# Kernel optimization log

Measured on AMD Instinct MI355X. Metric: run time of the kernel, lower is better.

## Reference

```python
import jax, jax.numpy as jnp
import numpy as np

EMBED_DIM = 1408
NUM_HEADS = 16
HEAD_DIM = EMBED_DIM // NUM_HEADS  # 88
SCALE = HEAD_DIM ** -0.5


def setup_inputs() -> dict:
    key = jax.random.key(0)
    k0, k1, k2, k3, k4 = jax.random.split(key, 5)
    B, S, D = 16, 577, EMBED_DIM
    hidden_states = jax.random.normal(k0, (B, S, D), dtype=jnp.float32)
    # fused QKV projection: [D, 3D] laid out as [q | k | v]
    w_qkv = jax.random.normal(k1, (D, 3 * D), dtype=jnp.float32) * (D ** -0.5)
    b_qkv = jax.random.normal(k2, (3 * D,), dtype=jnp.float32) * 0.02
    # output projection
    w_proj = jax.random.normal(k3, (D, D), dtype=jnp.float32) * (D ** -0.5)
    b_proj = jax.random.normal(k4, (D,), dtype=jnp.float32) * 0.02
    return {
        "hidden_states": hidden_states,
        "w_qkv": w_qkv,
        "b_qkv": b_qkv,
        "w_proj": w_proj,
        "b_proj": b_proj,
    }


def reference(hidden_states, w_qkv, b_qkv, w_proj, b_proj):
    B, S, D = hidden_states.shape
    H, Hd = NUM_HEADS, HEAD_DIM
    # fused QKV projection, then chunk along last dim (matches .chunk(3, -1))
    qkv = hidden_states @ w_qkv + b_qkv                      # [B, S, 3D]
    q, k, v = jnp.split(qkv, 3, axis=-1)                     # each [B, S, D]
    q = q.reshape(B, S, H, Hd)
    k = k.reshape(B, S, H, Hd)
    v = v.reshape(B, S, H, Hd)
    # scaled dot-product attention (no mask, no dropout at inference)
    scores = jnp.einsum("bqhd,bkhd->bhqk", q, k) * SCALE      # [B, H, S, S]
    probs = jax.nn.softmax(scores, axis=-1)
    out = jnp.einsum("bhqk,bkhd->bqhd", probs, v)             # [B, S, H, Hd]
    out = out.reshape(B, S, D)
    attn_output = out @ w_proj + b_proj                        # [B, S, D]
    return attn_output
```

## Files before the change

kernel.cpp:

```cpp
#include <hip/hip_runtime.h>
#include <cstddef>
#include <cstdint>

#define D_EMB   1408
#define NHEADS  16
#define HD      88
#define BATCH   16
#define SEQ     577
#define M_ROWS  (BATCH * SEQ)
#define N_QKV   (3 * D_EMB)
#define QKL_N   2816
#define SP      640
#define ATT_SCALE 0.10660035817780521f

#define QT 64
#define KT 64

typedef __attribute__((ext_vector_type(8))) short bf16x8;
typedef __attribute__((ext_vector_type(4))) float f32x4;
typedef unsigned short u16;

static __device__ __forceinline__ u16 f2bf(float x) {
  union { float f; unsigned u; } v; v.f = x;
  unsigned r = v.u + 0x7fff + ((v.u >> 16) & 1);
  return (u16)(r >> 16);
}
static __device__ __forceinline__ float bf2f(u16 h) {
  union { unsigned u; float f; } v; v.u = ((unsigned)h) << 16;
  return v.f;
}
static __device__ __forceinline__ void split_hl(float x, u16* hi, u16* lo) {
  u16 h = f2bf(x);
  *hi = h;
  *lo = f2bf(x - bf2f(h));
}

static __device__ __forceinline__ void async16(const u16* g, u16* l) {
  __builtin_amdgcn_global_load_lds(
      (const __attribute__((address_space(1))) unsigned int*)g,
      (__attribute__((address_space(3))) unsigned int*)l, 16, 0, 0);
}

__global__ __launch_bounds__(256)
void split_kernel(const float* __restrict__ X, u16* __restrict__ H,
                  u16* __restrict__ L, int n4) {
  int i = blockIdx.x * 256 + threadIdx.x;
  if (i >= n4) return;
  float4 v = ((const float4*)X)[i];
  ushort4 h, l;
  split_hl(v.x, &h.x, &l.x);
  split_hl(v.y, &h.y, &l.y);
  split_hl(v.z, &h.z, &l.z);
  split_hl(v.w, &h.w, &l.w);
  ((ushort4*)H)[i] = h;
  ((ushort4*)L)[i] = l;
}

__global__ __launch_bounds__(256)
void transpose_split_kernel(const float* __restrict__ W, u16* __restrict__ Th,
                            u16* __restrict__ Tl, int K, int N) {
  __shared__ float tile[32][33];
  const int n0 = blockIdx.x * 32, k0 = blockIdx.y * 32;
  const int tx = threadIdx.x & 31, ty = threadIdx.x >> 5;
#pragma unroll
  for (int i = 0; i < 4; ++i) {
    int k = ty + i * 8;
    tile[k][tx] = W[(size_t)(k0 + k) * N + n0 + tx];
  }
  __syncthreads();
#pragma unroll
  for (int i = 0; i < 4; ++i) {
    int n = ty + i * 8;
    float v = tile[tx][n];
    u16 h, l;
    split_hl(v, &h, &l);
    Th[(size_t)(n0 + n) * K + k0 + tx] = h;
    Tl[(size_t)(n0 + n) * K + k0 + tx] = l;
  }
}

__global__ __launch_bounds__(256)
void vtrans_kernel(const u16* __restrict__ qkvh, u16* __restrict__ vt) {
  __shared__ u16 tile[64][96];
  const int st = blockIdx.x, bh = blockIdx.y;
  const int b = bh >> 4, h = bh & 15;
  const int tid = threadIdx.x;
  const int s0 = st * 64;
  for (int idx = tid; idx < 64 * 22; idx += 256) {
    int j = idx / 22, c4 = (idx % 22) * 4;
    int s = s0 + j;
    ushort4 v = make_ushort4(0, 0, 0, 0);
    if (s < SEQ)
      v = *(const ushort4*)(qkvh + (size_t)(b * SEQ + s) * N_QKV + 2 * D_EMB + h * HD + c4);
    *(ushort4*)&tile[j][c4] = v;
  }
  if (tid < 64) {
    bf16x8 z = {0, 0, 0, 0, 0, 0, 0, 0};
    *(bf16x8*)&tile[tid][88] = z;
  }
  __syncthreads();
  for (int idx = tid; idx < 96 * 8; idx += 256) {
    int d = idx >> 3, c8 = (idx & 7) * 8;
    bf16x8 o;
#pragma unroll
    for (int e = 0; e < 8; ++e) o[e] = (short)tile[c8 + e][d];
    *(bf16x8*)(vt + ((size_t)bh * 96 + d) * SP + s0 + c8) = o;
  }
}

#define KDIM   1408
#define BMT    256
#define BNT    256
#define SLOT_E 32768
#define AS_H   0
#define AS_L   8192
#define BS_H   16384
#define BS_L   24576

#define STG_A(SLOTP, SSN)                                                 \
  {                                                                       \
    const int k0s = (SSN) * 32;                                           \
    u16* Ls = &Lds[SLOTP][0];                                             \
    async16(Ah + srcA0 + k0s, Ls + AS_H + ldsD0);                         \
    async16(Al + srcA0 + k0s, Ls + AS_L + ldsD0);                         \
    async16(Ah + srcA1 + k0s, Ls + AS_H + ldsD1);                         \
    async16(Al + srcA1 + k0s, Ls + AS_L + ldsD1);                         \
  }
#define STG_B(SLOTP, SSN)                                                 \
  {                                                                       \
    const int k0s = (SSN) * 32;                                           \
    u16* Ls = &Lds[SLOTP][0];                                             \
    async16(Bh + srcB0 + k0s, Ls + BS_H + ldsD0);                         \
    async16(Bl + srcB0 + k0s, Ls + BS_L + ldsD0);                         \
    async16(Bh + srcB1 + k0s, Ls + BS_H + ldsD1);                         \
    async16(Bl + srcB1 + k0s, Ls + BS_L + ldsD1);                         \
  }

#define MFMA3(ACC, AH, AL, BH, BL)                                                  \
  ACC = __builtin_amdgcn_mfma_f32_16x16x32_bf16(AH, BH, ACC, 0, 0, 0);              \
  ACC = __builtin_amdgcn_mfma_f32_16x16x32_bf16(AH, BL, ACC, 0, 0, 0);              \
  ACC = __builtin_amdgcn_mfma_f32_16x16x32_bf16(AL, BH, ACC, 0, 0, 0);

#define ROW_MFMA(I, AH, AL)                                               \
  MFMA3(acc[I][0], AH, AL, fbh0, fbl0)                                    \
  MFMA3(acc[I][1], AH, AL, fbh1, fbl1)                                    \
  MFMA3(acc[I][2], AH, AL, fbh2, fbl2)                                    \
  MFMA3(acc[I][3], AH, AL, fbh3, fbl3)

#define PH_SYNC                                                           \
  __builtin_amdgcn_s_barrier();                                           \
  asm volatile("s_waitcnt lgkmcnt(0)" ::: "memory");                      \
  __builtin_amdgcn_sched_barrier(0);

#define SLOT_RUN(PHYS, SSN, DO_STAGE, DO_VM)                              \
  {                                                                       \
    const u16* Lb = &Lds[PHYS][0];                                        \
    bf16x8 fbh0, fbh1, fbh2, fbh3, fbl0, fbl1, fbl2, fbl3;                \
    bf16x8 a0h, a0l, a1h, a1l;                                            \
                              \
    fbh0 = *(const bf16x8*)&Lb[BS_H + offB[0]];                           \
    fbh1 = *(const bf16x8*)&Lb[BS_H + offB[1]];                           \
    fbh2 = *(const bf16x8*)&Lb[BS_H + offB[2]];                           \
    fbh3 = *(const bf16x8*)&Lb[BS_H + offB[3]];                           \
    fbl0 = *(const bf16x8*)&Lb[BS_L + offB[0]];                           \
    fbl1 = *(const bf16x8*)&Lb[BS_L + offB[1]];                           \
    fbl2 = *(const bf16x8*)&Lb[BS_L + offB[2]];                           \
    fbl3 = *(const bf16x8*)&Lb[BS_L + offB[3]];                           \
    a0h = *(const bf16x8*)&Lb[AS_H + offA[0]];                            \
    a0l = *(const bf16x8*)&Lb[AS_L + offA[0]];                            \
    a1h = *(const bf16x8*)&Lb[AS_H + offA[1]];                            \
    a1l = *(const bf16x8*)&Lb[AS_L + offA[1]];                            \
    if (DO_STAGE) STG_A(PHYS ^ 1, SSN);                                   \
    PH_SYNC                                                               \
    __builtin_amdgcn_s_setprio(1);                                        \
    ROW_MFMA(0, a0h, a0l) ROW_MFMA(1, a1h, a1l)                           \
    __builtin_amdgcn_s_setprio(0);                                        \
    __builtin_amdgcn_s_barrier();                                         \
                                           \
    a0h = *(const bf16x8*)&Lb[AS_H + offA[2]];                            \
    a0l = *(const bf16x8*)&Lb[AS_L + offA[2]];                            \
    a1h = *(const bf16x8*)&Lb[AS_H + offA[3]];                            \
    a1l = *(const bf16x8*)&Lb[AS_L + offA[3]];                            \
    if (DO_STAGE) STG_B(PHYS ^ 1, SSN);                                   \
    PH_SYNC                                                               \
    __builtin_amdgcn_s_setprio(1);                                        \
    ROW_MFMA(2, a0h, a0l) ROW_MFMA(3, a1h, a1l)                           \
    __builtin_amdgcn_s_setprio(0);                                        \
    __builtin_amdgcn_s_barrier();                                         \
                                           \
    a0h = *(const bf16x8*)&Lb[AS_H + offA[4]];                            \
    a0l = *(const bf16x8*)&Lb[AS_L + offA[4]];                            \
    a1h = *(const bf16x8*)&Lb[AS_H + offA[5]];                            \
    a1l = *(const bf16x8*)&Lb[AS_L + offA[5]];                            \
    PH_SYNC                                                               \
    __builtin_amdgcn_s_setprio(1);                                        \
    ROW_MFMA(4, a0h, a0l) ROW_MFMA(5, a1h, a1l)                           \
    __builtin_amdgcn_s_setprio(0);                                        \
    __builtin_amdgcn_s_barrier();                                         \
                                           \
    a0h = *(const bf16x8*)&Lb[AS_H + offA[6]];                            \
    a0l = *(const bf16x8*)&Lb[AS_L + offA[6]];                            \
    a1h = *(const bf16x8*)&Lb[AS_H + offA[7]];                            \
    a1l = *(const bf16x8*)&Lb[AS_L + offA[7]];                            \
    PH_SYNC                                                               \
    __builtin_amdgcn_s_setprio(1);                                        \
    ROW_MFMA(6, a0h, a0l) ROW_MFMA(7, a1h, a1l)                           \
    __builtin_amdgcn_s_setprio(0);                                        \
    if (DO_VM) asm volatile("s_waitcnt vmcnt(0)" ::: "memory");           \
    __builtin_amdgcn_s_barrier();                                         \
  }

template <int MODE>
__global__ __launch_bounds__(512)
void gemm8p_kernel(const u16* __restrict__ Ah, const u16* __restrict__ Al,
                   const u16* __restrict__ Bh, const u16* __restrict__ Bl,
                   const float* __restrict__ bias,
                   float* __restrict__ Cf, u16* __restrict__ Ch, u16* __restrict__ Cl,
                   int M, int N, int NX) {
  const int lin  = blockIdx.x;
  const int xcd  = lin & 7;
  const int t    = lin >> 3;
  const int band = xcd + 8 * (t / NX);
  const int bm0  = band * BMT;
  if (bm0 >= M) return;
  const int bn0  = (t % NX) * BNT;

  __shared__ u16 Lds[2][SLOT_E];

  const int tid  = threadIdx.x;
  const int lane = tid & 63;
  const int w    = tid >> 6;
  const int quad = lane >> 4, lc = lane & 15;
  const int wm   = w >> 2, wn = w & 3;

  size_t srcA0, srcA1, srcB0, srcB1;
  int ldsD0, ldsD1;
  {
    int r0 = tid >> 2, q0 = tid & 3;
    int swz0 = (q0 ^ ((r0 >> 1) & 3)) * 8;
    int r1 = 128 + r0;
    int swz1 = (q0 ^ ((r1 >> 1) & 3)) * 8;
    int ra0 = bm0 + r0; if (ra0 > M - 1) ra0 = M - 1;
    int ra1 = bm0 + r1; if (ra1 > M - 1) ra1 = M - 1;
    srcA0 = (size_t)ra0 * KDIM + swz0;
    srcA1 = (size_t)ra1 * KDIM + swz1;
    int rb0 = bn0 + r0; if (rb0 > N - 1) rb0 = N - 1;
    int rb1 = bn0 + r1; if (rb1 > N - 1) rb1 = N - 1;
    srcB0 = (size_t)rb0 * KDIM + swz0;
    srcB1 = (size_t)rb1 * KDIM + swz1;
    ldsD0 = w * 512;
    ldsD1 = 4096 + w * 512;
  }

  int offA[8], offB[4];
  {
    const int qphys = quad ^ ((lc >> 1) & 3);
#pragma unroll
    for (int i = 0; i < 8; ++i)
      offA[i] = (wm * 128 + i * 16 + lc) * 32 + qphys * 8;
#pragma unroll
    for (int j = 0; j < 4; ++j)
      offB[j] = (wn * 64 + j * 16 + lc) * 32 + qphys * 8;
  }

  f32x4 acc[8][4];
#pragma unroll
  for (int i = 0; i < 8; ++i)
#pragma unroll
    for (int j = 0; j < 4; ++j) acc[i][j] = (f32x4){0.f, 0.f, 0.f, 0.f};

  STG_A(0, 0);
  STG_B(0, 0);
  asm volatile("s_waitcnt vmcnt(0)" ::: "memory");
  __builtin_amdgcn_s_barrier();

#pragma unroll 1
  for (int u = 0; u < 21; ++u) {
    SLOT_RUN(0, 2 * u + 1, true, true);
    SLOT_RUN(1, 2 * u + 2, true, true);
  }
  SLOT_RUN(0, 43, true, true);
  SLOT_RUN(1, 0, false, false);

#pragma unroll
  for (int j = 0; j < 4; ++j) {
    int col = bn0 + wn * 64 + j * 16 + lc;
    if (col < N) {
      float bj = bias[col];
#pragma unroll
      for (int i = 0; i < 8; ++i) {
#pragma unroll
        for (int rg = 0; rg < 4; ++rg) {
          int row = bm0 + wm * 128 + i * 16 + quad * 4 + rg;
          if (row < M) {
            float v = acc[i][j][rg] + bj;
            if (MODE == 0) {
              Cf[(size_t)row * N + col] = v;
            } else {
              u16 hh, ll;
              split_hl(v, &hh, &ll);
              Ch[(size_t)row * N + col] = hh;
              if (col < QKL_N) Cl[(size_t)row * QKL_N + col] = ll;
            }
          }
        }
      }
    }
  }
}

__global__ __launch_bounds__(256)
void attn_kernel2(const u16* __restrict__ qkvh, const u16* __restrict__ qkvl,
                  const u16* __restrict__ vt,
                  u16* __restrict__ outh, u16* __restrict__ outl) {
  __shared__ u16 Khi[KT][104];
  __shared__ u16 Klo[KT][104];
  __shared__ u16 Vs[96][72];
  __shared__ u16 Pb[QT][72];

  const int tid  = threadIdx.x;
  const int lane = tid & 63;
  const int wv   = tid >> 6;
  const int quad = lane >> 4;
  const int lc   = lane & 15;

  const int qt = blockIdx.x, h = blockIdx.y, b = blockIdx.z;
  const int q0 = qt * QT;

  if (tid < KT) {
    bf16x8 z = {0, 0, 0, 0, 0, 0, 0, 0};
    *(bf16x8*)&Khi[tid][88] = z;
    *(bf16x8*)&Klo[tid][88] = z;
  }

  bf16x8 qh[3], ql[3];
  {
    const bf16x8 z = {0, 0, 0, 0, 0, 0, 0, 0};
    int qrow = q0 + wv * 16 + lc;
    bool qv = qrow < SEQ;
    size_t bh_ = (size_t)(b * SEQ + (qv ? qrow : 0));
#pragma unroll
    for (int ks = 0; ks < 3; ++ks) {
      if (!qv || (ks == 2 && quad == 3)) {
        qh[ks] = z; ql[ks] = z;
      } else {
        qh[ks] = *(const bf16x8*)(qkvh + bh_ * N_QKV + h * HD + ks * 32 + quad * 8);
        ql[ks] = *(const bf16x8*)(qkvl + bh_ * QKL_N + h * HD + ks * 32 + quad * 8);
      }
    }
  }

  float mrow[4], lrow[4];
#pragma unroll
  for (int r = 0; r < 4; ++r) { mrow[r] = -INFINITY; lrow[r] = 0.f; }
  f32x4 oacc[6];
#pragma unroll
  for (int nn = 0; nn < 6; ++nn) oacc[nn] = (f32x4){0.f, 0.f, 0.f, 0.f};

  const u16* vsrc = vt + (size_t)(b * 16 + h) * 96 * SP;

  for (int kt = 0; kt < SP / KT; ++kt) {
    const int k0 = kt * KT;
    __syncthreads();

    for (int idx = tid; idx < KT * 22; idx += 256) {
      int j = idx / 22, c4 = (idx % 22) * 4;
      int s = k0 + j;
      ushort4 kh = make_ushort4(0, 0, 0, 0), kl = make_ushort4(0, 0, 0, 0);
      if (s < SEQ) {
        size_t rb = (size_t)(b * SEQ + s);
        kh = *(const ushort4*)(qkvh + rb * N_QKV + D_EMB + h * HD + c4);
        kl = *(const ushort4*)(qkvl + rb * QKL_N + D_EMB + h * HD + c4);
      }
      *(ushort4*)&Khi[j][c4] = kh;
      *(ushort4*)&Klo[j][c4] = kl;
    }
    for (int idx = tid; idx < 96 * 8; idx += 256) {
      int d = idx >> 3, c8 = (idx & 7) * 8;
      *(bf16x8*)&Vs[d][c8] = *(const bf16x8*)(vsrc + (size_t)d * SP + k0 + c8);
    }
    __syncthreads();

    f32x4 sc[4];
#pragma unroll
    for (int t = 0; t < 4; ++t) {
      f32x4 a = (f32x4){0.f, 0.f, 0.f, 0.f};
#pragma unroll
      for (int ks = 0; ks < 3; ++ks) {
        bf16x8 kh = *(const bf16x8*)&Khi[t * 16 + lc][ks * 32 + quad * 8];
        bf16x8 kl = *(const bf16x8*)&Klo[t * 16 + lc][ks * 32 + quad * 8];
        a = __builtin_amdgcn_mfma_f32_16x16x32_bf16(qh[ks], kh, a, 0, 0, 0);
        a = __builtin_amdgcn_mfma_f32_16x16x32_bf16(qh[ks], kl, a, 0, 0, 0);
        a = __builtin_amdgcn_mfma_f32_16x16x32_bf16(ql[ks], kh, a, 0, 0, 0);
      }
      sc[t] = a;
    }
#pragma unroll
    for (int t = 0; t < 4; ++t) {
      bool valid = (k0 + t * 16 + lc) < SEQ;
#pragma unroll
      for (int r = 0; r < 4; ++r)
        sc[t][r] = valid ? sc[t][r] * ATT_SCALE : -INFINITY;
    }

    float alpha[4];
#pragma unroll
    for (int r = 0; r < 4; ++r) {
      float v = fmaxf(fmaxf(sc[0][r], sc[1][r]), fmaxf(sc[2][r], sc[3][r]));
      v = fmaxf(v, __shfl_xor(v, 1));
      v = fmaxf(v, __shfl_xor(v, 2));
      v = fmaxf(v, __shfl_xor(v, 4));
      v = fmaxf(v, __shfl_xor(v, 8));
      float mnew = fmaxf(mrow[r], v);
      alpha[r] = expf(mrow[r] - mnew);
      mrow[r] = mnew;
      float s = 0.f;
#pragma unroll
      for (int t = 0; t < 4; ++t) {
        float p = expf(sc[t][r] - mnew);
        sc[t][r] = p;
        s += p;
      }
      s += __shfl_xor(s, 1);
      s += __shfl_xor(s, 2);
      s += __shfl_xor(s, 4);
      s += __shfl_xor(s, 8);
      lrow[r] = lrow[r] * alpha[r] + s;
    }
#pragma unroll
    for (int t = 0; t < 4; ++t)
#pragma unroll
      for (int r = 0; r < 4; ++r)
        Pb[wv * 16 + quad * 4 + r][t * 16 + lc] = f2bf(sc[t][r]);
#pragma unroll
    for (int nn = 0; nn < 6; ++nn)
#pragma unroll
      for (int r = 0; r < 4; ++r) oacc[nn][r] *= alpha[r];
    __syncthreads();

    bf16x8 p0 = *(const bf16x8*)&Pb[wv * 16 + lc][quad * 8];
    bf16x8 p1 = *(const bf16x8*)&Pb[wv * 16 + lc][32 + quad * 8];
#pragma unroll
    for (int nn = 0; nn < 6; ++nn) {
      bf16x8 v0 = *(const bf16x8*)&Vs[nn * 16 + lc][quad * 8];
      bf16x8 v1 = *(const bf16x8*)&Vs[nn * 16 + lc][32 + quad * 8];
      oacc[nn] = __builtin_amdgcn_mfma_f32_16x16x32_bf16(p0, v0, oacc[nn], 0, 0, 0);
      oacc[nn] = __builtin_amdgcn_mfma_f32_16x16x32_bf16(p1, v1, oacc[nn], 0, 0, 0);
    }
  }

#pragma unroll
  for (int r = 0; r < 4; ++r) {
    int s = q0 + wv * 16 + quad * 4 + r;
    if (s < SEQ) {
      float inv = 1.f / lrow[r];
      size_t base = (size_t)(b * SEQ + s) * D_EMB + h * HD;
#pragma unroll
      for (int nn = 0; nn < 6; ++nn) {
        int d = nn * 16 + lc;
        if (d < HD) {
          float v = oacc[nn][r] * inv;
          u16 hh, ll;
          split_hl(v, &hh, &ll);
          outh[base + d] = hh;
          outl[base + d] = ll;
        }
      }
    }
  }
}

extern "C" void kernel_launch(void* const* d_in, const int* in_sizes, int n_in,
                              void* d_out, int out_size, void* d_ws, size_t ws_size,
                              hipStream_t stream) {
  const float* hs    = (const float*)d_in[0];
  const float* wqkv  = (const float*)d_in[1];
  const float* bqkv  = (const float*)d_in[2];
  const float* wproj = (const float*)d_in[3];
  const float* bproj = (const float*)d_in[4];
  float* out = (float*)d_out;

  u16* qkvH = (u16*)d_ws;
  u16* qkvL = qkvH + (size_t)M_ROWS * N_QKV;
  u16* hsH  = qkvL + (size_t)M_ROWS * QKL_N;
  u16* hsL  = hsH + (size_t)M_ROWS * D_EMB;
  u16* vt   = hsL + (size_t)M_ROWS * D_EMB;
  u16* wtH  = vt;
  u16* wtL  = wtH + (size_t)N_QKV * D_EMB;
  u16* attnH = hsH;
  u16* attnL = hsL;

  {
    int n4 = (M_ROWS * D_EMB) / 4;
    split_kernel<<<(n4 + 255) / 256, 256, 0, stream>>>(hs, hsH, hsL, n4);
  }
  {
    dim3 g(N_QKV / 32, D_EMB / 32);
    transpose_split_kernel<<<g, 256, 0, stream>>>(wqkv, wtH, wtL, D_EMB, N_QKV);
  }
  {
    gemm8p_kernel<1><<<17 * 40, 512, 0, stream>>>(hsH, hsL, wtH, wtL, bqkv,
                                                  nullptr, qkvH, qkvL,
                                                  M_ROWS, N_QKV, 17);
  }
  {
    dim3 g(SP / 64, BATCH * NHEADS);
    vtrans_kernel<<<g, 256, 0, stream>>>(qkvH, vt);
  }
  {
    dim3 g(SP / QT, NHEADS, BATCH);
    attn_kernel2<<<g, 256, 0, stream>>>(qkvH, qkvL, vt, attnH, attnL);
  }
  {
    dim3 g(D_EMB / 32, D_EMB / 32);
    transpose_split_kernel<<<g, 256, 0, stream>>>(wproj, wtH, wtL, D_EMB, D_EMB);
  }
  {
    gemm8p_kernel<0><<<6 * 40, 512, 0, stream>>>(attnH, attnL, wtH, wtL, bproj,
                                                 out, nullptr, nullptr,
                                                 M_ROWS, D_EMB, 6);
  }
}
```

Baseline: 867.0 us.

## Collapse GEMM slot phases into two halves with fewer barriers and reordered MFMAs

Restructures the per-slot inner loop of the split-bf16 GEMM. The four barrier-separated phases become two halves: A fragments for four row-groups are loaded at once, both A and B stages for the next slot are issued together, and the second half's A loads overlap the first half's MFMAs. The three-term MFMA sequence is reordered so consecutive MFMAs target different accumulators, avoiding back-to-back dependent issue. This removes most intra-slot s_barrier calls at the cost of more live fragment registers and less lock-step between waves.

```diff
diff --git a/kernel.cpp b/kernel.cpp
--- a/kernel.cpp
+++ b/kernel.cpp
@@ -136,28 +136,25 @@
     async16(Bl + srcB1 + k0s, Ls + BS_L + ldsD1);                         \
   }
 
-#define MFMA3(ACC, AH, AL, BH, BL)                                                  \
-  ACC = __builtin_amdgcn_mfma_f32_16x16x32_bf16(AH, BH, ACC, 0, 0, 0);              \
-  ACC = __builtin_amdgcn_mfma_f32_16x16x32_bf16(AH, BL, ACC, 0, 0, 0);              \
-  ACC = __builtin_amdgcn_mfma_f32_16x16x32_bf16(AL, BH, ACC, 0, 0, 0);
-
-#define ROW_MFMA(I, AH, AL)                                               \
-  MFMA3(acc[I][0], AH, AL, fbh0, fbl0)                                    \
-  MFMA3(acc[I][1], AH, AL, fbh1, fbl1)                                    \
-  MFMA3(acc[I][2], AH, AL, fbh2, fbl2)                                    \
-  MFMA3(acc[I][3], AH, AL, fbh3, fbl3)
-
-#define PH_SYNC                                                           \
-  __builtin_amdgcn_s_barrier();                                           \
-  asm volatile("s_waitcnt lgkmcnt(0)" ::: "memory");                      \
-  __builtin_amdgcn_sched_barrier(0);
+#define ROW_MFMA(I, AH, AL)                                                              \
+  acc[I][0] = __builtin_amdgcn_mfma_f32_16x16x32_bf16(AH, fbh0, acc[I][0], 0, 0, 0);     \
+  acc[I][1] = __builtin_amdgcn_mfma_f32_16x16x32_bf16(AH, fbh1, acc[I][1], 0, 0, 0);     \
+  acc[I][2] = __builtin_amdgcn_mfma_f32_16x16x32_bf16(AH, fbh2, acc[I][2], 0, 0, 0);     \
+  acc[I][3] = __builtin_amdgcn_mfma_f32_16x16x32_bf16(AH, fbh3, acc[I][3], 0, 0, 0);     \
+  acc[I][0] = __builtin_amdgcn_mfma_f32_16x16x32_bf16(AH, fbl0, acc[I][0], 0, 0, 0);     \
+  acc[I][1] = __builtin_amdgcn_mfma_f32_16x16x32_bf16(AH, fbl1, acc[I][1], 0, 0, 0);     \
+  acc[I][2] = __builtin_amdgcn_mfma_f32_16x16x32_bf16(AH, fbl2, acc[I][2], 0, 0, 0);     \
+  acc[I][3] = __builtin_amdgcn_mfma_f32_16x16x32_bf16(AH, fbl3, acc[I][3], 0, 0, 0);     \
+  acc[I][0] = __builtin_amdgcn_mfma_f32_16x16x32_bf16(AL, fbh0, acc[I][0], 0, 0, 0);     \
+  acc[I][1] = __builtin_amdgcn_mfma_f32_16x16x32_bf16(AL, fbh1, acc[I][1], 0, 0, 0);     \
+  acc[I][2] = __builtin_amdgcn_mfma_f32_16x16x32_bf16(AL, fbh2, acc[I][2], 0, 0, 0);     \
+  acc[I][3] = __builtin_amdgcn_mfma_f32_16x16x32_bf16(AL, fbh3, acc[I][3], 0, 0, 0);
 
 #define SLOT_RUN(PHYS, SSN, DO_STAGE, DO_VM)                              \
   {                                                                       \
     const u16* Lb = &Lds[PHYS][0];                                        \
     bf16x8 fbh0, fbh1, fbh2, fbh3, fbl0, fbl1, fbl2, fbl3;                \
-    bf16x8 a0h, a0l, a1h, a1l;                                            \
-                              \
+    bf16x8 fa0h, fa0l, fa1h, fa1l, fa2h, fa2l, fa3h, fa3l;                \
     fbh0 = *(const bf16x8*)&Lb[BS_H + offB[0]];                           \
     fbh1 = *(const bf16x8*)&Lb[BS_H + offB[1]];                           \
     fbh2 = *(const bf16x8*)&Lb[BS_H + offB[2]];                           \
@@ -166,45 +163,35 @@
     fbl1 = *(const bf16x8*)&Lb[BS_L + offB[1]];                           \
     fbl2 = *(const bf16x8*)&Lb[BS_L + offB[2]];                           \
     fbl3 = *(const bf16x8*)&Lb[BS_L + offB[3]];                           \
-    a0h = *(const bf16x8*)&Lb[AS_H + offA[0]];                            \
-    a0l = *(const bf16x8*)&Lb[AS_L + offA[0]];                            \
-    a1h = *(const bf16x8*)&Lb[AS_H + offA[1]];                            \
-    a1l = *(const bf16x8*)&Lb[AS_L + offA[1]];                            \
-    if (DO_STAGE) STG_A(PHYS ^ 1, SSN);                                   \
-    PH_SYNC                                                               \
+    fa0h = *(const bf16x8*)&Lb[AS_H + offA[0]];                           \
+    fa0l = *(const bf16x8*)&Lb[AS_L + offA[0]];                           \
+    fa1h = *(const bf16x8*)&Lb[AS_H + offA[1]];                           \
+    fa1l = *(const bf16x8*)&Lb[AS_L + offA[1]];                           \
+    fa2h = *(const bf16x8*)&Lb[AS_H + offA[2]];                           \
+    fa2l = *(const bf16x8*)&Lb[AS_L + offA[2]];                           \
+    fa3h = *(const bf16x8*)&Lb[AS_H + offA[3]];                           \
+    fa3l = *(const bf16x8*)&Lb[AS_L + offA[3]];                           \
+    if (DO_STAGE) { STG_A(PHYS ^ 1, SSN); STG_B(PHYS ^ 1, SSN); }         \
+    asm volatile("s_waitcnt lgkmcnt(0)" ::: "memory");                    \
+    __builtin_amdgcn_sched_barrier(0);                                    \
+    bf16x8 ga0h, ga0l, ga1h, ga1l, ga2h, ga2l, ga3h, ga3l;                \
+    ga0h = *(const bf16x8*)&Lb[AS_H + offA[4]];                           \
+    ga0l = *(const bf16x8*)&Lb[AS_L + offA[4]];                           \
+    ga1h = *(const bf16x8*)&Lb[AS_H + offA[5]];                           \
+    ga1l = *(const bf16x8*)&Lb[AS_L + offA[5]];                           \
+    ga2h = *(const bf16x8*)&Lb[AS_H + offA[6]];                           \
+    ga2l = *(const bf16x8*)&Lb[AS_L + offA[6]];                           \
+    ga3h = *(const bf16x8*)&Lb[AS_H + offA[7]];                           \
+    ga3l = *(const bf16x8*)&Lb[AS_L + offA[7]];                           \
     __builtin_amdgcn_s_setprio(1);                                        \
-    ROW_MFMA(0, a0h, a0l) ROW_MFMA(1, a1h, a1l)                           \
+    ROW_MFMA(0, fa0h, fa0l) ROW_MFMA(1, fa1h, fa1l)                       \
+    ROW_MFMA(2, fa2h, fa2l) ROW_MFMA(3, fa3h, fa3l)                       \
     __builtin_amdgcn_s_setprio(0);                                        \
-    __builtin_amdgcn_s_barrier();                                         \
-                                           \
-    a0h = *(const bf16x8*)&Lb[AS_H + offA[2]];                            \
-    a0l = *(const bf16x8*)&Lb[AS_L + offA[2]];                            \
-    a1h = *(const bf16x8*)&Lb[AS_H + offA[3]];                            \
-    a1l = *(const bf16x8*)&Lb[AS_L + offA[3]];                            \
-    if (DO_STAGE) STG_B(PHYS ^ 1, SSN);                                   \
-    PH_SYNC                                                               \
+    asm volatile("s_waitcnt lgkmcnt(0)" ::: "memory");                    \
+    __builtin_amdgcn_sched_barrier(0);                                    \
     __builtin_amdgcn_s_setprio(1);                                        \
-    ROW_MFMA(2, a0h, a0l) ROW_MFMA(3, a1h, a1l)                           \
-    __builtin_amdgcn_s_setprio(0);                                        \
-    __builtin_amdgcn_s_barrier();                                         \
-                                           \
-    a0h = *(const bf16x8*)&Lb[AS_H + offA[4]];                            \
-    a0l = *(const bf16x8*)&Lb[AS_L + offA[4]];                            \
-    a1h = *(const bf16x8*)&Lb[AS_H + offA[5]];                            \
-    a1l = *(const bf16x8*)&Lb[AS_L + offA[5]];                            \
-    PH_SYNC                                                               \
-    __builtin_amdgcn_s_setprio(1);                                        \
-    ROW_MFMA(4, a0h, a0l) ROW_MFMA(5, a1h, a1l)                           \
-    __builtin_amdgcn_s_setprio(0);                                        \
-    __builtin_amdgcn_s_barrier();                                         \
-                                           \
-    a0h = *(const bf16x8*)&Lb[AS_H + offA[6]];                            \
-    a0l = *(const bf16x8*)&Lb[AS_L + offA[6]];                            \
-    a1h = *(const bf16x8*)&Lb[AS_H + offA[7]];                            \
-    a1l = *(const bf16x8*)&Lb[AS_L + offA[7]];                            \
-    PH_SYNC                                                               \
-    __builtin_amdgcn_s_setprio(1);                                        \
-    ROW_MFMA(6, a0h, a0l) ROW_MFMA(7, a1h, a1l)                           \
+    ROW_MFMA(4, ga0h, ga0l) ROW_MFMA(5, ga1h, ga1l)                       \
+    ROW_MFMA(6, ga2h, ga2l) ROW_MFMA(7, ga3h, ga3l)                       \
     __builtin_amdgcn_s_setprio(0);                                        \
     if (DO_VM) asm volatile("s_waitcnt vmcnt(0)" ::: "memory");           \
     __builtin_amdgcn_s_barrier();                                         \
```

Result: slower. 995.2 us (+14.8%).
